# Kernel tuning notes

Measured on AMD Instinct MI355X. Metric: run time of the kernel, lower is better.

The kernel has to match this reference:

```python
import jax, jax.numpy as jnp
import numpy as np

B_, N_, D_ = 8, 1024, 64
H_, DH_ = 4, 16
DI_, DS_, DTR_ = 128, 64, 4
MAXP = 512


def _ln(x, w, b, eps=1e-5):
    m = jnp.mean(x, -1, keepdims=True)
    v = jnp.mean((x - m) ** 2, -1, keepdims=True)
    return (x - m) * jax.lax.rsqrt(v + eps) * w + b


def _attn(x, drop_mask, Wq, Wkv, Wo, bo, rel_emb):
    b, n, d = x.shape
    scale = DH_ ** -0.5
    q = (x @ Wq).reshape(b, n, H_, DH_).transpose(0, 2, 1, 3)
    kv = x @ Wkv
    k = kv[..., :d].reshape(b, n, H_, DH_).transpose(0, 2, 1, 3)
    v = kv[..., d:].reshape(b, n, H_, DH_).transpose(0, 2, 1, 3)
    dots = jnp.einsum('bhid,bhjd->bhij', q, k) * scale
    seq = jnp.arange(n)
    dist = jnp.clip(seq[:, None] - seq[None, :], -MAXP, MAXP) + MAXP
    rpe = rel_emb[dist]  # (n, n, DH_)
    dots = dots + jnp.einsum('bhid,ijd->bhij', q, rpe) * scale
    # stochastic key drop: Bernoulli(0.3) positions get -1e12
    dots = dots + drop_mask.astype(dots.dtype) * (-1e12)
    attn = jax.nn.softmax(dots, axis=-1)
    out = jnp.einsum('bhij,bhjd->bhid', attn, v)
    out = out.transpose(0, 2, 1, 3).reshape(b, n, H_ * DH_)
    return out @ Wo + bo


def _mamba(x, W_in, conv_w, conv_b, W_xproj, W_dt, b_dt, A_log, Dm, W_out):
    b, n, _ = x.shape
    xz = x @ W_in                      # (b, n, 2*DI_)
    u, z = xz[..., :DI_], xz[..., DI_:]
    uc = u.transpose(0, 2, 1)          # (b, DI_, n)
    uc = jax.lax.conv_general_dilated(
        uc, conv_w[:, None, :], (1,), ((3, 0),),
        feature_group_count=DI_, dimension_numbers=('NCH', 'OIH', 'NCH'))
    uc = uc + conv_b[None, :, None]
    u = jax.nn.silu(uc).transpose(0, 2, 1)  # (b, n, DI_)
    xdb = u @ W_xproj                  # (b, n, DTR_+2*DS_)
    dt = jax.nn.softplus(xdb[..., :DTR_] @ W_dt + b_dt)  # (b, n, DI_)
    Bm = xdb[..., DTR_:DTR_ + DS_]
    Cm = xdb[..., DTR_ + DS_:]
    A = -jnp.exp(A_log)                # (DI_, DS_)

    def step(h, inp):
        dt_t, B_t, C_t, u_t = inp      # (b,DI_),(b,DS_),(b,DS_),(b,DI_)
        dA = jnp.exp(dt_t[..., None] * A)
        h = h * dA + (dt_t * u_t)[..., None] * B_t[:, None, :]
        y = jnp.einsum('bds,bs->bd', h, C_t)
        return h, y

    h0 = jnp.zeros((b, DI_, DS_), x.dtype)
    xs = (dt.transpose(1, 0, 2), Bm.transpose(1, 0, 2),
          Cm.transpose(1, 0, 2), u.transpose(1, 0, 2))
    _, ys = jax.lax.scan(step, h0, xs)
    y = ys.transpose(1, 0, 2) + u * Dm
    y = y * jax.nn.silu(z)
    return y @ W_out


def _rmsgn(x, gamma, eps=1e-5, groups=4):
    shp = x.shape
    dpg = shp[-1] // groups
    xg = x.reshape(shp[:-1] + (groups, dpg))
    rms = jnp.sqrt(jnp.sum(xg * xg, -1, keepdims=True)) * (dpg ** -0.5)
    return (xg / (rms + eps)).reshape(shp) * gamma


def _ff1(x, c1_w, c1_b, d1_w, d1_b):
    # SwiGLUConvDeconv1d(64, 256, kernel=4, shift=1); x: (b, s2, 64)
    s2 = x.shape[1]
    xc = x.transpose(0, 2, 1)
    xc = jnp.pad(xc, ((0, 0), (0, 0), (3, 3)))
    xc = jax.lax.conv_general_dilated(
        xc, c1_w, (1,), 'VALID', dimension_numbers=('NCH', 'OIH', 'NCH'))
    xc = xc + c1_b[None, :, None]
    gate = jax.nn.silu(xc[:, 256:, :])
    xc = xc[:, :256, :] * gate
    # ConvTranspose1d stride 1 == conv with flipped kernel, full padding
    w = jnp.flip(d1_w, -1).transpose(1, 0, 2)  # (64, 256, 4)
    xc = jax.lax.conv_general_dilated(
        xc, w, (1,), ((3, 3),), dimension_numbers=('NCH', 'OIH', 'NCH'))
    xc = xc + d1_b[None, :, None]
    out = xc.transpose(0, 2, 1)
    return out[:, 3:3 + s2, :]


def _forward(x, drop_mask, ln1_w, ln1_b, Wq, Wkv, Wo, bo, rel_emb,
             ln2_w, ln2_b, W_in, conv_w, conv_b, W_xproj, W_dt, b_dt,
             A_log, Dm, W_out, gamma, c1_w, c1_b, d1_w, d1_b, ln3_w, ln3_b):
    xt = _ln(x, ln1_w, ln1_b)
    xt = _attn(xt, drop_mask, Wq, Wkv, Wo, bo, rel_emb) + x
    x = x + xt  # dropout p=0 -> identity (faithful to original residual math)
    xt = _ln(x, ln2_w, ln2_b)
    m = _mamba(xt, W_in, conv_w, conv_b, W_xproj, W_dt, b_dt, A_log, Dm, W_out)
    m = jnp.where(m >= 0, m, 0.01 * m)  # leaky_relu
    m = _rmsgn(m, gamma)
    m = m + 0.5 * _ff1(m, c1_w, c1_b, d1_w, d1_b)
    x = x + m
    return _ln(x, ln3_w, ln3_b)


def setup_inputs() -> dict:
    ks = jax.random.split(jax.random.key(0), 16)
    g = lambda i, shp, s: jax.random.normal(ks[i], shp, dtype=jnp.float32) * s
    A_log = jnp.log(jnp.tile(jnp.arange(1, DS_ + 1, dtype=jnp.float32)[None, :], (DI_, 1)))
    return {
        'x': jax.random.normal(ks[0], (B_, N_, D_), dtype=jnp.float32),
        'drop_mask': jax.random.bernoulli(ks[1], 0.3, (B_, H_, N_, N_)),
        'ln1_w': jnp.ones((D_,), jnp.float32), 'ln1_b': jnp.zeros((D_,), jnp.float32),
        'Wq': g(2, (D_, D_), 0.1), 'Wkv': g(3, (D_, 2 * D_), 0.1),
        'Wo': g(4, (D_, D_), 0.1), 'bo': jnp.zeros((D_,), jnp.float32),
        'rel_emb': g(5, (2 * MAXP + 1, DH_), 0.02),
        'ln2_w': jnp.ones((D_,), jnp.float32), 'ln2_b': jnp.zeros((D_,), jnp.float32),
        'W_in': g(6, (D_, 2 * DI_), 0.1),
        'conv_w': g(7, (DI_, 4), 0.2), 'conv_b': jnp.zeros((DI_,), jnp.float32),
        'W_xproj': g(8, (DI_, DTR_ + 2 * DS_), 0.1),
        'W_dt': g(9, (DTR_, DI_), 0.1), 'b_dt': jnp.zeros((DI_,), jnp.float32),
        'A_log': A_log, 'Dm': jnp.ones((DI_,), jnp.float32),
        'W_out': g(10, (DI_, D_), 0.1),
        'gamma': jnp.ones((D_,), jnp.float32),
        'c1_w': g(11, (512, 64, 4), 0.1), 'c1_b': jnp.zeros((512,), jnp.float32),
        'd1_w': g(12, (256, 64, 4), 0.1), 'd1_b': jnp.zeros((64,), jnp.float32),
        'ln3_w': jnp.ones((D_,), jnp.float32), 'ln3_b': jnp.zeros((D_,), jnp.float32),
    }


def reference(x, drop_mask, ln1_w, ln1_b, Wq, Wkv, Wo, bo, rel_emb,
              ln2_w, ln2_b, W_in, conv_w, conv_b, W_xproj, W_dt, b_dt,
              A_log, Dm, W_out, gamma, c1_w, c1_b, d1_w, d1_b, ln3_w, ln3_b):
    return _forward(x, drop_mask, ln1_w, ln1_b, Wq, Wkv, Wo, bo, rel_emb,
                    ln2_w, ln2_b, W_in, conv_w, conv_b, W_xproj, W_dt, b_dt,
                    A_log, Dm, W_out, gamma, c1_w, c1_b, d1_w, d1_b, ln3_w, ln3_b)
```

## Files before the change

kernel.cpp:

```cpp
#include <hip/hip_runtime.h>
#include <hip/hip_fp16.h>
#include <math.h>


__device__ __forceinline__ float wsum64(float v){
#pragma unroll
  for(int m=32;m>0;m>>=1) v += __shfl_xor(v, m, 64);
  return v;
}
__device__ __forceinline__ float wmax64(float v){
#pragma unroll
  for(int m=32;m>0;m>>=1) v = fmaxf(v, __shfl_xor(v, m, 64));
  return v;
}
__device__ __forceinline__ float silu_f(float x){ return x / (1.f + __expf(-x)); }
__device__ __forceinline__ float rfl_f(float x){
  return __int_as_float(__builtin_amdgcn_readfirstlane(__float_as_int(x)));
}

__global__ __launch_bounds__(256) void k_ln1_qkv(
    const float* __restrict__ x, const float* __restrict__ w1, const float* __restrict__ b1,
    const float* __restrict__ Wq, const float* __restrict__ Wkv,
    const float* __restrict__ rel, const float* __restrict__ c1w,
    const int* __restrict__ dmask,
    float* __restrict__ qb, float2* __restrict__ kvT,
    float* __restrict__ relT, float* __restrict__ c1wT,
    unsigned long long* __restrict__ mask64){
  int tid = threadIdx.x;
  int bi = blockIdx.x >> 1;
  if (blockIdx.x & 1){
    size_t base = (size_t)bi * 16384;
    const int* dp = dmask + base;
    unsigned long long* mp = mask64 + (base >> 6);
#pragma unroll 4
    for(int r=0;r<64;++r){
      int m = dp[r*256 + tid];
      unsigned long long bal = __ballot(m != 0);
      if ((tid & 63) == 0) mp[r*4 + (tid >> 6)] = bal;
    }
    return;
  }
  int lane = tid & 63, warp = tid >> 6;
  int token = bi*4 + warp;
  __shared__ float xt[4][64];
  float xv = x[(size_t)token*64 + lane];
  float mean = wsum64(xv) * 0.015625f;
  float dlt = xv - mean;
  float var = wsum64(dlt*dlt) * 0.015625f;
  float xn = dlt * rsqrtf(var + 1e-5f) * w1[lane] + b1[lane];
  xt[warp][lane] = xn;
  __syncthreads();
  float aq=0.f, ak=0.f, av=0.f;
#pragma unroll 4
  for(int dd=0; dd<64; ++dd){
    float xd = xt[warp][dd];
    aq += xd * Wq[dd*64 + lane];
    ak += xd * Wkv[dd*128 + lane];
    av += xd * Wkv[dd*128 + 64 + lane];
  }
  int b = token >> 10, i = token & 1023;
  int h = lane >> 4, dh = lane & 15;
  size_t o  = (((size_t)(b*4 + h))*1024 + i)*16 + dh;
  size_t oT = (((size_t)(b*4 + h))*16 + dh)*1024 + i;
  qb[o]=aq;
  kvT[oT] = make_float2(ak, av);

  if (bi < 65){
    int idx = bi*256 + tid;
    if (idx < 16*1025){
      int c = idx / 1025;
      int d = idx - c*1025;
      relT[idx] = rel[d*16 + c];
    }
  } else if (bi < 577){
    int idx = (bi-65)*256 + tid;
    int row = idx >> 9;
    int ii  = idx & 511;
    c1wT[idx] = c1w[(size_t)ii*256 + row];
  }
}

__global__ __launch_bounds__(256) void k_kmax(
    const float2* __restrict__ kvT, float* __restrict__ Kmax){
  int tid = threadIdx.x;
  int bh = blockIdx.x;
  const float2* base = kvT + (size_t)bh*16*1024;
  float mx = 0.f;
#pragma unroll
  for(int r=0;r<4;++r){
    int j = tid + 256*r;
    float ss = 0.f;
#pragma unroll
    for(int c=0;c<16;++c){ float2 kv = base[c*1024 + j]; ss += kv.x*kv.x; }
    mx = fmaxf(mx, ss);
  }
  mx = wmax64(mx);
  __shared__ float red[4];
  int lane = tid&63, wv = tid>>6;
  if(lane==0) red[wv]=mx;
  __syncthreads();
  if(tid==0) Kmax[bh] = sqrtf(fmaxf(fmaxf(red[0],red[1]),fmaxf(red[2],red[3])));
}

__global__ __launch_bounds__(256, 2) void k_attn(
    const float* __restrict__ qb, const float2* __restrict__ kvT,
    const unsigned long long* __restrict__ mask64, const float* __restrict__ relT,
    const float* __restrict__ Kmax, float* __restrict__ attn_raw){
  int tid = threadIdx.x;
  int lane = tid & 63;
  int wvu  = __builtin_amdgcn_readfirstlane(tid >> 6);
  int wg   = blockIdx.x;
  int xcd  = wg & 7;
  int slot = wg >> 3;
  int bh   = xcd*4 + (slot >> 6);
  int i0   = (slot & 63) * 16;
  int b = bh >> 2, h = bh & 3;
  int R0 = wvu*4, R1 = R0+1, R2 = R0+2, R3 = R0+3;

  __shared__ __align__(16) __half Gc[16][1040];
  __shared__ float kvX[2][16][64];
  __shared__ float kvY[2][16][64];
  __shared__ float qs[16][16];
  __shared__ float G0s[16], G1024s[16];
  __shared__ float gmS[16];
  __shared__ float Ms[16];
  __shared__ float sums[16];

  {
    int r = tid >> 4, c = tid & 15;
    qs[r][c] = qb[((size_t)bh*1024 + i0 + r)*16 + c] * 0.25f;
  }
  __syncthreads();

  float q0[16], q1[16], q2[16], q3[16];
#pragma unroll
  for(int c=0;c<16;++c){
    q0[c]=rfl_f(qs[R0][c]); q1[c]=rfl_f(qs[R1][c]);
    q2[c]=rfl_f(qs[R2][c]); q3[c]=rfl_f(qs[R3][c]);
  }

  const float2* kvb = kvT + (size_t)bh*16*1024;
  float2 st[4];
#define LOADREGS(CH) do{ int _j0=(CH)*64;                                   \
    _Pragma("unroll")                                                       \
    for(int k=0;k<4;++k){ int idx=tid+256*k; int c=idx>>6, jl=idx&63;       \
      st[k]=kvb[c*1024 + _j0 + jl]; } }while(0)
#define WRITEB(NB) do{                                                      \
    _Pragma("unroll")                                                       \
    for(int k=0;k<4;++k){ int idx=tid+256*k; int c=idx>>6, jl=idx&63;       \
      kvX[NB][c][jl]=st[k].x; kvY[NB][c][jl]=st[k].y; } }while(0)

  LOADREGS(0);

#pragma unroll 1
  for(int bb=0; bb<17; ++bb){
    int d = lane + 64*bb;
    if (d <= 1024){
      float rl[16];
#pragma unroll
      for(int c=0;c<16;++c) rl[c] = relT[c*1025 + d];
      float g0=0.f, g1=0.f, g2=0.f, g3=0.f;
#pragma unroll
      for(int c=0;c<16;++c){
        float rc = rl[c];
        g0 += q0[c]*rc; g1 += q1[c]*rc; g2 += q2[c]*rc; g3 += q3[c]*rc;
      }
      if (d == 0){ G0s[R0]=g0; G0s[R1]=g1; G0s[R2]=g2; G0s[R3]=g3; }
      else if (d == 1024){ G1024s[R0]=g0; G1024s[R1]=g1; G1024s[R2]=g2; G1024s[R3]=g3; }
      else {
        int base = i0 + 512 - d;
        int j0r = base + R0;
        if (j0r+0 >= 0 && j0r+0 < 1024) Gc[R0][j0r+0] = __float2half_rn(g0);
        if (j0r+1 >= 0 && j0r+1 < 1024) Gc[R1][j0r+1] = __float2half_rn(g1);
        if (j0r+2 >= 0 && j0r+2 < 1024) Gc[R2][j0r+2] = __float2half_rn(g2);
        if (j0r+3 >= 0 && j0r+3 < 1024) Gc[R3][j0r+3] = __float2half_rn(g3);
      }
    }
  }
  __syncthreads();
  {
    const unsigned long long* mrow = mask64 + ((size_t)bh*1024 + i0)*16;
#pragma unroll 1
    for(int r=0;r<16;++r){
      float g0 = G0s[r], g1 = G1024s[r];
      int lo = i0 + r - 512;
      int hi = i0 + r + 512;
#pragma unroll
      for(int p=0;p<4;++p){
        int j = tid + 256*p;
        unsigned long long w = mrow[r*16 + (j>>6)];
        float g;
        if (j >= hi) g = g0;
        else if (j <= lo) g = g1;
        else g = __half2float(Gc[r][j]);
        if ((w >> (j & 63)) & 1ULL) g = -60000.f;
        Gc[r][j] = __float2half_rn(g);
      }
    }
  }
  __syncthreads();
  {
    int r = tid >> 4, l4 = tid & 15;
    float gm = -3.0e38f;
#pragma unroll
    for(int k=0;k<64;++k) gm = fmaxf(gm, __half2float(Gc[r][l4 + 16*k]));
#pragma unroll
    for(int m=1;m<16;m<<=1) gm = fmaxf(gm, __shfl_xor(gm, m, 64));
    if (l4 == 0) gmS[r] = gm;
  }
  __syncthreads();
  if (tid < 16){
    float qn = 0.f;
#pragma unroll
    for(int c=0;c<16;++c) qn += qs[tid][c]*qs[tid][c];
    Ms[tid] = gmS[tid] + sqrtf(qn)*Kmax[bh];
  }
  __syncthreads();

  float M0 = rfl_f(Ms[R0]), M1 = rfl_f(Ms[R1]);
  float M2 = rfl_f(Ms[R2]), M3 = rfl_f(Ms[R3]);

  float s0=0.f, s1=0.f, s2=0.f, s3=0.f;
  float a0[16], a1[16], a2[16], a3[16];
#pragma unroll
  for(int c=0;c<16;++c){ a0[c]=0.f; a1[c]=0.f; a2[c]=0.f; a3[c]=0.f; }

  WRITEB(0);
  LOADREGS(1);
  __syncthreads();
  int cur = 0;

#pragma unroll 1
  for(int ch=0; ch<16; ++ch){
    int j = ch*64 + lane;
    float sv0 = __half2float(Gc[R0][j]), sv1 = __half2float(Gc[R1][j]);
    float sv2 = __half2float(Gc[R2][j]), sv3 = __half2float(Gc[R3][j]);
#pragma unroll
    for(int c=0;c<16;++c){
      float kxc = kvX[cur][c][lane];
      sv0 += q0[c]*kxc; sv1 += q1[c]*kxc; sv2 += q2[c]*kxc; sv3 += q3[c]*kxc;
    }
    float p0 = __expf(sv0 - M0), p1 = __expf(sv1 - M1);
    float p2 = __expf(sv2 - M2), p3 = __expf(sv3 - M3);
    s0 += p0; s1 += p1; s2 += p2; s3 += p3;
#pragma unroll
    for(int c=0;c<16;++c){
      float vyc = kvY[cur][c][lane];
      a0[c] += p0*vyc; a1[c] += p1*vyc; a2[c] += p2*vyc; a3[c] += p3*vyc;
    }
    if (ch < 15){
      WRITEB(cur^1);
      if (ch < 14) LOADREGS(ch+2);
    }
    __syncthreads();
    cur ^= 1;
  }
#undef LOADREGS
#undef WRITEB

  s0 = wsum64(s0); s1 = wsum64(s1); s2 = wsum64(s2); s3 = wsum64(s3);
#pragma unroll
  for(int c=0;c<16;++c){
    float x0 = a0[c]; x0 += __shfl_xor(x0,32,64); x0 += __shfl_xor(x0,16,64); a0[c] = x0;
    float x1 = a1[c]; x1 += __shfl_xor(x1,32,64); x1 += __shfl_xor(x1,16,64); a1[c] = x1;
    float x2 = a2[c]; x2 += __shfl_xor(x2,32,64); x2 += __shfl_xor(x2,16,64); a2[c] = x2;
    float x3 = a3[c]; x3 += __shfl_xor(x3,32,64); x3 += __shfl_xor(x3,16,64); a3[c] = x3;
  }
  __syncthreads();
  float* red = (float*)&Gc[0][0];
  if (lane < 16){
#pragma unroll
    for(int c=0;c<16;++c){
      red[R0*272 + lane*17 + c] = a0[c];
      red[R1*272 + lane*17 + c] = a1[c];
      red[R2*272 + lane*17 + c] = a2[c];
      red[R3*272 + lane*17 + c] = a3[c];
    }
  }
  if (lane == 0){ sums[R0]=s0; sums[R1]=s1; sums[R2]=s2; sums[R3]=s3; }
  __syncthreads();
  {
    int row = tid >> 4, c = tid & 15;
    float tot = 0.f;
#pragma unroll
    for(int g=0; g<16; ++g) tot += red[row*272 + g*17 + c];
    attn_raw[((size_t)b*1024 + i0 + row)*64 + h*16 + c] = tot / sums[row];
  }
}

__global__ __launch_bounds__(256) void k_post_attn(
    const float* __restrict__ x, const float* __restrict__ attn_raw,
    const float* __restrict__ Wo, const float* __restrict__ bo,
    const float* __restrict__ ln2w, const float* __restrict__ ln2b,
    const float* __restrict__ W_in,
    float* __restrict__ x2, float* __restrict__ u0, float* __restrict__ zsarr){
  int tid = threadIdx.x;
  int lane = tid & 63, wv = tid >> 6;
  int tok0 = blockIdx.x * 16;
  __shared__ float arS[16][64];
  __shared__ float lnS[16][64];
  for(int l = tid; l < 1024; l += 256)
    arS[l >> 6][l & 63] = attn_raw[(size_t)tok0*64 + l];
  __syncthreads();
#pragma unroll 1
  for(int tt = 0; tt < 4; ++tt){
    int tl = wv*4 + tt;
    int token = tok0 + tl;
    float acc = bo[lane];
#pragma unroll 4
    for(int dd = 0; dd < 64; ++dd) acc += arS[tl][dd] * Wo[dd*64 + lane];
    float t = 2.f*x[(size_t)token*64 + lane] + acc;
    x2[(size_t)token*64 + lane] = t;
    float mean = wsum64(t)*0.015625f;
    float dlt = t - mean;
    float var = wsum64(dlt*dlt)*0.015625f;
    lnS[tl][lane] = dlt*rsqrtf(var+1e-5f)*ln2w[lane] + ln2b[lane];
  }
  __syncthreads();
  int oc = tid;
  float w[64];
#pragma unroll
  for(int dd = 0; dd < 64; ++dd) w[dd] = W_in[dd*256 + oc];
  const float4* lnS4 = (const float4*)&lnS[0][0];
#pragma unroll 1
  for(int tl = 0; tl < 16; ++tl){
    float acc = 0.f;
#pragma unroll
    for(int d4 = 0; d4 < 16; ++d4){
      float4 l4 = lnS4[tl*16 + d4];
      acc += l4.x*w[4*d4] + l4.y*w[4*d4+1] + l4.z*w[4*d4+2] + l4.w*w[4*d4+3];
    }
    int token = tok0 + tl;
    if (oc < 128) u0[(size_t)token*128 + oc] = acc;
    else          zsarr[(size_t)token*128 + (oc-128)] = silu_f(acc);
  }
}

__global__ __launch_bounds__(256) void k_conv_proj(
    const float* __restrict__ u0, const float* __restrict__ conv_w, const float* __restrict__ conv_b,
    const float* __restrict__ W_xproj, const float* __restrict__ W_dt, const float* __restrict__ b_dt,
    float* __restrict__ uarr, float* __restrict__ Bmp, float* __restrict__ Cmp, float* __restrict__ dtarr){
  int sub = threadIdx.x >> 7, c = threadIdx.x & 127;
  int token = blockIdx.x*2 + sub;
  int b = token >> 10, i = token & 1023;
  __shared__ float us[2][128];
  __shared__ float dtin[2][4];
  float acc = conv_b[c];
#pragma unroll
  for(int k2=0;k2<4;++k2){
    int t2 = i - 3 + k2;
    if (t2 >= 0) acc += u0[((size_t)b*1024 + t2)*128 + c]*conv_w[c*4+k2];
  }
  float uv = silu_f(acc);
  uarr[(size_t)token*128 + c] = uv;
  us[sub][c] = uv;
  __syncthreads();
  float accA = 0.f, accB = 0.f;
  int cB = 128 + (c & 3);
#pragma unroll 4
  for(int dd=0; dd<128; ++dd){
    float xd = us[sub][dd];
    accA += xd * W_xproj[dd*132 + c];
    accB += xd * W_xproj[dd*132 + cB];
  }
  if (c < 4){ dtin[sub][c] = accA; Cmp[(size_t)token*64 + 60 + c] = accB; }
  else if (c < 68) Bmp[(size_t)token*64 + (c-4)] = accA;
  else             Cmp[(size_t)token*64 + (c-68)] = accA;
  __syncthreads();
  float dv = b_dt[c];
#pragma unroll
  for(int r2=0;r2<4;++r2) dv += dtin[sub][r2]*W_dt[r2*128 + c];
  dv = fmaxf(dv, 0.f) + log1pf(expf(-fabsf(dv)));
  dtarr[(size_t)token*128 + c] = dv;
}

__global__ __launch_bounds__(256) void k_scan_a(
    const float* __restrict__ dtarr, const float* __restrict__ uarr,
    const float* __restrict__ Bmp, const float* __restrict__ A_log,
    float* __restrict__ Parr, float* __restrict__ Rarr){
  int lane = threadIdx.x & 63, warp = threadIdx.x >> 6;
  int wgid = blockIdx.x;
  int b = wgid & 7;
  int slot = wgid >> 3;
  int d = slot & 127;
  int c = (slot >> 7)*4 + warp;
  size_t pw = (size_t)b*1024 + d*8 + c;
  float A = -expf(A_log[d*64 + lane]);
  int tb = c*128;
  const float* dtp = dtarr + ((size_t)b*1024 + tb)*128 + d;
  const float* up  = uarr  + ((size_t)b*1024 + tb)*128 + d;
  const float* Bp  = Bmp   + ((size_t)b*1024 + tb)*64 + lane;
  float R = 0.f, sdt = 0.f;
  for(int t0=0; t0<128; t0+=8){
    float dtc[8], uc[8], Bc[8];
#pragma unroll
    for(int r=0;r<8;++r){
      dtc[r]=dtp[(size_t)(t0+r)*128]; uc[r]=up[(size_t)(t0+r)*128]; Bc[r]=Bp[(size_t)(t0+r)*64];
    }
#pragma unroll
    for(int r=0;r<8;++r){
      float dt = dtc[r];
      R = R*__expf(dt*A) + dt*uc[r]*Bc[r];
      sdt += dt;
    }
  }
  Parr[pw*64 + lane] = __expf(sdt*A);
  Rarr[pw*64 + lane] = R;
}

__global__ __launch_bounds__(256) void k_scan_c(
    const float* __restrict__ dtarr, const float* __restrict__ uarr,
    const float* __restrict__ Bmp, const float* __restrict__ Cmp,
    const float* __restrict__ zsarr, const float* __restrict__ A_log,
    const float* __restrict__ Dm, const float* __restrict__ Parr,
    const float* __restrict__ Rarr, float* __restrict__ ymp){
  int lane = threadIdx.x & 63, warp = threadIdx.x >> 6;
  int wgid = blockIdx.x;
  int b = wgid & 7;
  int slot = wgid >> 3;
  int d = slot & 127;
  int c = (slot >> 7)*4 + warp;
  size_t pbase = (size_t)b*1024 + d*8;
  float A = -expf(A_log[d*64 + lane]);
  float Dv = Dm[d];
  float h = 0.f;
#pragma unroll 1
  for(int cp=0; cp<c; ++cp){
    float P = Parr[(pbase+cp)*64 + lane];
    float R = Rarr[(pbase+cp)*64 + lane];
    h = h*P + R;
  }
  int tb = c*128;
  const float* dtp = dtarr + ((size_t)b*1024 + tb)*128 + d;
  const float* up  = uarr  + ((size_t)b*1024 + tb)*128 + d;
  const float* zp  = zsarr + ((size_t)b*1024 + tb)*128 + d;
  const float* Bp  = Bmp   + ((size_t)b*1024 + tb)*64 + lane;
  const float* Cp  = Cmp   + ((size_t)b*1024 + tb)*64 + lane;
  float* yp        = ymp   + ((size_t)b*1024 + tb)*128 + d;
  for(int t0=0; t0<128; t0+=8){
    float dtc[8], uc[8], Bc[8], Cc[8], zc[8];
#pragma unroll
    for(int r=0;r<8;++r){
      dtc[r]=dtp[(size_t)(t0+r)*128]; uc[r]=up[(size_t)(t0+r)*128];
      Bc[r]=Bp[(size_t)(t0+r)*64];    Cc[r]=Cp[(size_t)(t0+r)*64];
      zc[r]=zp[(size_t)(t0+r)*128];
    }
    float hc[8];
#pragma unroll
    for(int r=0;r<8;++r){
      float dt = dtc[r];
      h = h*__expf(dt*A) + dt*uc[r]*Bc[r];
      hc[r] = h*Cc[r];
    }
    float y[8];
#pragma unroll
    for(int r=0;r<8;++r) y[r] = wsum64(hc[r]);
    if (lane==0){
#pragma unroll
      for(int r=0;r<8;++r) yp[(size_t)(t0+r)*128] = (y[r] + uc[r]*Dv)*zc[r];
    }
  }
}

__global__ __launch_bounds__(256) void k_wout(
    const float* __restrict__ ymp, const float* __restrict__ W_out,
    const float* __restrict__ gamma, float* __restrict__ marr){
  int lane = threadIdx.x & 63, warp = threadIdx.x >> 6;
  int token = blockIdx.x*4 + warp;
  __shared__ float ys[4][128];
  ys[warp][lane]      = ymp[(size_t)token*128 + lane];
  ys[warp][lane+64]   = ymp[(size_t)token*128 + 64 + lane];
  __syncthreads();
  float acc = 0.f;
#pragma unroll 4
  for(int dd=0; dd<128; ++dd) acc += ys[warp][dd]*W_out[dd*64 + lane];
  acc = acc >= 0.f ? acc : 0.01f*acc;
  float ss = acc*acc;
#pragma unroll
  for(int m=1;m<16;m<<=1) ss += __shfl_xor(ss, m, 64);
  float rms = sqrtf(ss)*0.25f;
  marr[(size_t)token*64 + lane] = acc/(rms + 1e-5f)*gamma[lane];
}

__global__ __launch_bounds__(256) void k_h2(
    const float* __restrict__ marr, const float* __restrict__ c1wT,
    const float* __restrict__ c1b, float* __restrict__ h2){
  int b = blockIdx.y;
  int t0 = blockIdx.x * 16;
  int tid = threadIdx.x;
  __shared__ float ms[19][64];
  for(int l = tid; l < 19*64; l += 256){
    int row = l >> 6, cc = l & 63;
    int t = t0 - 3 + row;
    ms[row][cc] = (t >= 0 && t < 1024) ? marr[((size_t)b*1024 + t)*64 + cc] : 0.f;
  }
  __syncthreads();
  int i = tid;
  float acc1[16], acc2[16];
#pragma unroll
  for(int tl=0;tl<16;++tl){ acc1[tl]=0.f; acc2[tl]=0.f; }
  for(int cc=0; cc<64; ++cc){
    float mv[19];
#pragma unroll
    for(int r2=0;r2<19;++r2) mv[r2] = ms[r2][cc];
    const float* wr = c1wT + (size_t)cc*4*512;
    float wa0 = wr[      i], wa1 = wr[ 512+i], wa2 = wr[1024+i], wa3 = wr[1536+i];
    float wg0 = wr[  256+i], wg1 = wr[ 768+i], wg2 = wr[1280+i], wg3 = wr[1792+i];
#pragma unroll
    for(int tl=0; tl<16; ++tl){
      acc1[tl] += wa0*mv[tl+0] + wa1*mv[tl+1] + wa2*mv[tl+2] + wa3*mv[tl+3];
      acc2[tl] += wg0*mv[tl+0] + wg1*mv[tl+1] + wg2*mv[tl+2] + wg3*mv[tl+3];
    }
  }
  float bb1 = c1b[i], bb2 = c1b[i+256];
#pragma unroll
  for(int tl=0; tl<16; ++tl){
    int t = t0 + tl;
    if (t < 1027){
      float o1 = acc1[tl] + bb1;
      float o2 = acc2[tl] + bb2;
      h2[((size_t)b*1027 + t)*256 + i] = o1 * silu_f(o2);
    }
  }
}

__global__ __launch_bounds__(256) void k_ff_final(
    const float* __restrict__ h2, const float* __restrict__ d1w, const float* __restrict__ d1b,
    const float* __restrict__ x2, const float* __restrict__ marr,
    const float* __restrict__ ln3w, const float* __restrict__ ln3b,
    float* __restrict__ out){
  int b = blockIdx.y;
  int s0 = blockIdx.x * 16;
  int tid = threadIdx.x;
  int o = tid & 63, sg = tid >> 6;
  __shared__ float hs[19][256];
  for(int l = tid; l < 19*256; l += 256){
    int row = l >> 8, cc = l & 255;
    hs[row][cc] = h2[((size_t)b*1027 + s0 + row)*256 + cc];
  }
  __syncthreads();
  int sl = sg*4;
  float acc0=0.f, acc1=0.f, acc2=0.f, acc3=0.f;
  const float4* wb = (const float4*)d1w + o;
#pragma unroll 2
  for(int i2=0; i2<256; ++i2){
    float4 wv = wb[(size_t)i2*64];
    float h0=hs[sl+0][i2], h1=hs[sl+1][i2], h2v=hs[sl+2][i2], h3=hs[sl+3][i2];
    float h4=hs[sl+4][i2], h5=hs[sl+5][i2], h6=hs[sl+6][i2];
    acc0 += h0*wv.w + h1*wv.z + h2v*wv.y + h3*wv.x;
    acc1 += h1*wv.w + h2v*wv.z + h3*wv.y + h4*wv.x;
    acc2 += h2v*wv.w + h3*wv.z + h4*wv.y + h5*wv.x;
    acc3 += h3*wv.w + h4*wv.z + h5*wv.y + h6*wv.x;
  }
  float accs[4] = {acc0, acc1, acc2, acc3};
  float bo_ = d1b[o];
#pragma unroll
  for(int r=0;r<4;++r){
    int s = s0 + sl + r;
    size_t idx = ((size_t)b*1024 + s)*64 + o;
    float tot = x2[idx] + marr[idx] + 0.5f*(accs[r] + bo_);
    float mean = wsum64(tot)*0.015625f;
    float dlt = tot - mean;
    float var = wsum64(dlt*dlt)*0.015625f;
    out[idx] = dlt*rsqrtf(var+1e-5f)*ln3w[o] + ln3b[o];
  }
}

extern "C" void kernel_launch(void* const* d_in, const int* in_sizes, int n_in,
                              void* d_out, int out_size, void* d_ws, size_t ws_size,
                              hipStream_t stream){
  const float* x       = (const float*)d_in[0];
  const int*   dmask   = (const int*)  d_in[1];
  const float* ln1w    = (const float*)d_in[2];
  const float* ln1b    = (const float*)d_in[3];
  const float* Wq      = (const float*)d_in[4];
  const float* Wkv     = (const float*)d_in[5];
  const float* Wo      = (const float*)d_in[6];
  const float* bo      = (const float*)d_in[7];
  const float* rel     = (const float*)d_in[8];
  const float* ln2w    = (const float*)d_in[9];
  const float* ln2b    = (const float*)d_in[10];
  const float* W_in    = (const float*)d_in[11];
  const float* conv_w  = (const float*)d_in[12];
  const float* conv_b  = (const float*)d_in[13];
  const float* W_xproj = (const float*)d_in[14];
  const float* W_dt    = (const float*)d_in[15];
  const float* b_dt    = (const float*)d_in[16];
  const float* A_log   = (const float*)d_in[17];
  const float* Dm      = (const float*)d_in[18];
  const float* W_out   = (const float*)d_in[19];
  const float* gamma   = (const float*)d_in[20];
  const float* c1w     = (const float*)d_in[21];
  const float* c1b     = (const float*)d_in[22];
  const float* d1w     = (const float*)d_in[23];
  const float* d1b     = (const float*)d_in[24];
  const float* ln3w    = (const float*)d_in[25];
  const float* ln3b    = (const float*)d_in[26];
  float* outp = (float*)d_out;

  float* ws = (float*)d_ws;
  float* qb       = ws;
  float* kvT      = qb      + 524288;
  float* attn_raw = kvT     + 1048576;
  float* x2       = attn_raw+ 524288;
  float* u0       = x2      + 524288;
  float* zsarr    = u0      + 1048576;
  float* uarr     = zsarr   + 1048576;
  float* dtarr    = uarr    + 1048576;
  float* Bmp      = dtarr   + 1048576;
  float* Cmp      = Bmp     + 524288;
  float* ymp      = Cmp     + 524288;
  float* marr     = ymp     + 1048576;
  float* h2       = marr    + 524288;
  float* relT     = h2      + 2103296;
  float* c1wT     = relT    + 16400;
  float* Parr     = c1wT    + 131072;
  float* Rarr     = Parr    + 524288;
  float* Kmaxa    = Rarr    + 524288;

  unsigned long long* mask64 = (unsigned long long*)h2;

  k_ln1_qkv  <<<4096, 256, 0, stream>>>(x, ln1w, ln1b, Wq, Wkv, rel, c1w, dmask,
                                        qb, (float2*)kvT, relT, c1wT, mask64);
  k_kmax     <<<32, 256, 0, stream>>>((const float2*)kvT, Kmaxa);
  k_attn     <<<2048, 256, 0, stream>>>(qb, (const float2*)kvT, mask64, relT, Kmaxa, attn_raw);
  k_post_attn<<<512, 256, 0, stream>>>(x, attn_raw, Wo, bo, ln2w, ln2b, W_in, x2, u0, zsarr);
  k_conv_proj<<<4096, 256, 0, stream>>>(u0, conv_w, conv_b, W_xproj, W_dt, b_dt, uarr, Bmp, Cmp, dtarr);
  k_scan_a   <<<2048, 256, 0, stream>>>(dtarr, uarr, Bmp, A_log, Parr, Rarr);
  k_scan_c   <<<2048, 256, 0, stream>>>(dtarr, uarr, Bmp, Cmp, zsarr, A_log, Dm, Parr, Rarr, ymp);
  k_wout     <<<2048, 256, 0, stream>>>(ymp, W_out, gamma, marr);
  k_h2       <<<dim3(65,8), 256, 0, stream>>>(marr, c1wT, c1b, h2);
  k_ff_final <<<dim3(64,8), 256, 0, stream>>>(h2, d1w, d1b, x2, marr, ln3w, ln3b, outp);
}
```

Measured before the change: 714.9 us.

## Fuse key-norm max into QKV kernel via atomics and vectorize mask packing

Result: no change. 719.8 us (+0.7%).

```diff
diff --git a/kernel.cpp b/kernel.cpp
--- a/kernel.cpp
+++ b/kernel.cpp
@@ -25,18 +25,41 @@
     const int* __restrict__ dmask,
     float* __restrict__ qb, float2* __restrict__ kvT,
     float* __restrict__ relT, float* __restrict__ c1wT,
-    unsigned long long* __restrict__ mask64){
+    unsigned long long* __restrict__ mask64, unsigned* __restrict__ KmaxSq){
   int tid = threadIdx.x;
   int bi = blockIdx.x >> 1;
   if (blockIdx.x & 1){
     size_t base = (size_t)bi * 16384;
-    const int* dp = dmask + base;
+    const int4* dp4 = (const int4*)(dmask + base);
     unsigned long long* mp = mask64 + (base >> 6);
-#pragma unroll 4
-    for(int r=0;r<64;++r){
-      int m = dp[r*256 + tid];
-      unsigned long long bal = __ballot(m != 0);
-      if ((tid & 63) == 0) mp[r*4 + (tid >> 6)] = bal;
+    int lane = tid & 63, wv = tid >> 6;
+    int li = (lane & 15) * 4;
+#pragma unroll 1
+    for(int p=0; p<4; ++p){
+      int4 v0 = dp4[p*1024 + tid*4 + 0];
+      int4 v1 = dp4[p*1024 + tid*4 + 1];
+      int4 v2 = dp4[p*1024 + tid*4 + 2];
+      int4 v3 = dp4[p*1024 + tid*4 + 3];
+      unsigned m = 0;
+      m |= (v0.x!=0) ? 1u<<0  : 0u;  m |= (v0.y!=0) ? 1u<<1  : 0u;
+      m |= (v0.z!=0) ? 1u<<2  : 0u;  m |= (v0.w!=0) ? 1u<<3  : 0u;
+      m |= (v1.x!=0) ? 1u<<4  : 0u;  m |= (v1.y!=0) ? 1u<<5  : 0u;
+      m |= (v1.z!=0) ? 1u<<6  : 0u;  m |= (v1.w!=0) ? 1u<<7  : 0u;
+      m |= (v2.x!=0) ? 1u<<8  : 0u;  m |= (v2.y!=0) ? 1u<<9  : 0u;
+      m |= (v2.z!=0) ? 1u<<10 : 0u;  m |= (v2.w!=0) ? 1u<<11 : 0u;
+      m |= (v3.x!=0) ? 1u<<12 : 0u;  m |= (v3.y!=0) ? 1u<<13 : 0u;
+      m |= (v3.z!=0) ? 1u<<14 : 0u;  m |= (v3.w!=0) ? 1u<<15 : 0u;
+      unsigned s0 = __shfl(m, li+0, 64);
+      unsigned s1 = __shfl(m, li+1, 64);
+      unsigned s2 = __shfl(m, li+2, 64);
+      unsigned s3 = __shfl(m, li+3, 64);
+      if (lane < 16){
+        unsigned long long word = (unsigned long long)s0
+          | ((unsigned long long)s1 << 16)
+          | ((unsigned long long)s2 << 32)
+          | ((unsigned long long)s3 << 48);
+        mp[p*64 + wv*16 + lane] = word;
+      }
     }
     return;
   }
@@ -65,6 +88,13 @@
   qb[o]=aq;
   kvT[oT] = make_float2(ak, av);
 
+  float kk = ak*ak;
+  kk += __shfl_xor(kk, 1, 64);
+  kk += __shfl_xor(kk, 2, 64);
+  kk += __shfl_xor(kk, 4, 64);
+  kk += __shfl_xor(kk, 8, 64);
+  if (dh == 0) atomicMax(KmaxSq + (b*4 + h), __float_as_uint(kk));
+
   if (bi < 65){
     int idx = bi*256 + tid;
     if (idx < 16*1025){
@@ -80,32 +110,10 @@
   }
 }
 
-__global__ __launch_bounds__(256) void k_kmax(
-    const float2* __restrict__ kvT, float* __restrict__ Kmax){
-  int tid = threadIdx.x;
-  int bh = blockIdx.x;
-  const float2* base = kvT + (size_t)bh*16*1024;
-  float mx = 0.f;
-#pragma unroll
-  for(int r=0;r<4;++r){
-    int j = tid + 256*r;
-    float ss = 0.f;
-#pragma unroll
-    for(int c=0;c<16;++c){ float2 kv = base[c*1024 + j]; ss += kv.x*kv.x; }
-    mx = fmaxf(mx, ss);
-  }
-  mx = wmax64(mx);
-  __shared__ float red[4];
-  int lane = tid&63, wv = tid>>6;
-  if(lane==0) red[wv]=mx;
-  __syncthreads();
-  if(tid==0) Kmax[bh] = sqrtf(fmaxf(fmaxf(red[0],red[1]),fmaxf(red[2],red[3])));
-}
-
 __global__ __launch_bounds__(256, 2) void k_attn(
     const float* __restrict__ qb, const float2* __restrict__ kvT,
     const unsigned long long* __restrict__ mask64, const float* __restrict__ relT,
-    const float* __restrict__ Kmax, float* __restrict__ attn_raw){
+    const unsigned* __restrict__ KmaxSq, float* __restrict__ attn_raw){
   int tid = threadIdx.x;
   int lane = tid & 63;
   int wvu  = __builtin_amdgcn_readfirstlane(tid >> 6);
@@ -213,7 +221,8 @@
     float qn = 0.f;
 #pragma unroll
     for(int c=0;c<16;++c) qn += qs[tid][c]*qs[tid][c];
-    Ms[tid] = gmS[tid] + sqrtf(qn)*Kmax[bh];
+    float km = sqrtf(__uint_as_float(KmaxSq[bh]));
+    Ms[tid] = gmS[tid] + sqrtf(qn)*km;
   }
   __syncthreads();
 
@@ -619,11 +628,12 @@
   float* Kmaxa    = Rarr    + 524288;
 
   unsigned long long* mask64 = (unsigned long long*)h2;
-
+  unsigned* KmaxSqU = (unsigned*)Kmaxa;
+
+  hipMemsetAsync(KmaxSqU, 0, 32*sizeof(unsigned), stream);
   k_ln1_qkv  <<<4096, 256, 0, stream>>>(x, ln1w, ln1b, Wq, Wkv, rel, c1w, dmask,
-                                        qb, (float2*)kvT, relT, c1wT, mask64);
-  k_kmax     <<<32, 256, 0, stream>>>((const float2*)kvT, Kmaxa);
-  k_attn     <<<2048, 256, 0, stream>>>(qb, (const float2*)kvT, mask64, relT, Kmaxa, attn_raw);
+                                        qb, (float2*)kvT, relT, c1wT, mask64, KmaxSqU);
+  k_attn     <<<2048, 256, 0, stream>>>(qb, (const float2*)kvT, mask64, relT, KmaxSqU, attn_raw);
   k_post_attn<<<512, 256, 0, stream>>>(x, attn_raw, Wo, bo, ln2w, ln2b, W_in, x2, u0, zsarr);
   k_conv_proj<<<4096, 256, 0, stream>>>(u0, conv_w, conv_b, W_xproj, W_dt, b_dt, uarr, Bmp, Cmp, dtarr);
   k_scan_a   <<<2048, 256, 0, stream>>>(dtarr, uarr, Bmp, A_log, Parr, Rarr);
```
